# Performance work log

Hardware: AMD Instinct MI355X
Metric: run time of the kernel (lower is better)

## Reference

```python
import jax, jax.numpy as jnp
import numpy as np

EMBED = 1024
HEADS = 16
HEAD_DIM = EMBED // HEADS


def setup_inputs() -> dict:
    key = jax.random.key(0)
    kx, kq, kk, kv, ko = jax.random.split(key, 5)
    s = 1.0 / np.sqrt(EMBED)
    return {
        "x": jax.random.normal(kx, (4, 2048, EMBED), dtype=jnp.float32),
        "Wq": jax.random.uniform(kq, (EMBED, EMBED), jnp.float32, -s, s),
        "Wk": jax.random.uniform(kk, (EMBED, EMBED), jnp.float32, -s, s),
        "Wv": jax.random.uniform(kv, (EMBED, EMBED), jnp.float32, -s, s),
        "Wo": jax.random.uniform(ko, (EMBED, EMBED), jnp.float32, -s, s),
    }


def reference(x, Wq, Wk, Wv, Wo):
    B, S, E = x.shape
    # nn.Linear computes x @ W.T; weights stored as (out, in)
    q = (x @ Wq.T).reshape(B, S, HEADS, HEAD_DIM).transpose(0, 2, 1, 3)  # [B,H,S,D]
    k = (x @ Wk.T).reshape(B, S, HEADS, HEAD_DIM).transpose(0, 2, 1, 3)
    v = (x @ Wv.T).reshape(B, S, HEADS, HEAD_DIM).transpose(0, 2, 1, 3)
    scores = jnp.einsum("bhsd,bhtd->bhst", q, k) / np.sqrt(HEAD_DIM)  # [B,H,S,S]
    causal = jnp.triu(jnp.ones((S, S), dtype=bool), k=1)
    scores = jnp.where(causal[None, None], -jnp.inf, scores)
    probs = jax.nn.softmax(scores, axis=-1)  # dropout_rate=0 -> identity
    attn = jnp.einsum("bhst,bhtd->bhsd", probs, v)  # [B,H,S,D]
    attn = attn.transpose(0, 2, 1, 3).reshape(B, S, E)
    return attn @ Wo.T
```

## Files before the change

### kernel.cpp

```cpp
#include <hip/hip_runtime.h>

#define EMB 1024
#define NHEADS 16
#define HD 64
#define BATCH 4
#define SEQ 2048
#define MTOK (BATCH*SEQ)

typedef __bf16 bf16x8 __attribute__((ext_vector_type(8)));
typedef __bf16 bf16x4 __attribute__((ext_vector_type(4)));
typedef float  f32x4  __attribute__((ext_vector_type(4)));

#define MFMA16(a,b,c) __builtin_amdgcn_mfma_f32_16x16x32_bf16(a,b,c,0,0,0)

__device__ __forceinline__ void gload_lds16(const __bf16* g, __bf16* l) {
    __builtin_amdgcn_global_load_lds(
        (__attribute__((address_space(1))) void*)(g),
        (__attribute__((address_space(3))) void*)(l), 16, 0, 0);
}

__global__ void cvt_f32_bf16(const float* __restrict__ in, __bf16* __restrict__ out, int n) {
    int i = (blockIdx.x * blockDim.x + threadIdx.x) * 4;
    if (i < n) {
        float4 v = *(const float4*)(in + i);
        bf16x4 o = { (__bf16)v.x, (__bf16)v.y, (__bf16)v.z, (__bf16)v.w };
        *(bf16x4*)(out + i) = o;
    }
}

__device__ __forceinline__ void gemm_bt_body(
    const __bf16* __restrict__ A, const __bf16* __restrict__ Bw,
    int tileM, int tileN, __bf16* As, __bf16* Bs, f32x4 acc[4][4])
{
    const int tid   = threadIdx.x;
    const int w     = tid >> 6;
    const int lane  = tid & 63;
    const int mlane = lane & 15;
    const int quad  = lane >> 4;
    const int wm    = (w >> 1) * 64;
    const int wn    = (w & 1) * 64;

    const f32x4 fzero = {0.f, 0.f, 0.f, 0.f};
    #pragma unroll
    for (int mi = 0; mi < 4; ++mi)
        #pragma unroll
        for (int ni = 0; ni < 4; ++ni) acc[mi][ni] = fzero;

    for (int kt = 0; kt < EMB; kt += 32) {
        #pragma unroll
        for (int i = 0; i < 2; ++i) {
            int cbase = i * 256 + w * 64;
            int c  = cbase + lane;
            int m  = c >> 2;
            int dq = (c & 3) ^ ((m >> 1) & 3);
            gload_lds16(A  + (size_t)(tileM + m) * EMB + kt + dq * 8, As + cbase * 8);
            gload_lds16(Bw + (size_t)(tileN + m) * EMB + kt + dq * 8, Bs + cbase * 8);
        }
        asm volatile("s_waitcnt vmcnt(0)" ::: "memory");
        __syncthreads();

        bf16x8 af[4], bfr[4];
        #pragma unroll
        for (int mi = 0; mi < 4; ++mi) {
            int row = wm + mi * 16 + mlane;
            af[mi] = *(const bf16x8*)(As + row * 32 + ((quad ^ ((row >> 1) & 3)) * 8));
        }
        #pragma unroll
        for (int ni = 0; ni < 4; ++ni) {
            int row = wn + ni * 16 + mlane;
            bfr[ni] = *(const bf16x8*)(Bs + row * 32 + ((quad ^ ((row >> 1) & 3)) * 8));
        }
        #pragma unroll
        for (int mi = 0; mi < 4; ++mi)
            #pragma unroll
            for (int ni = 0; ni < 4; ++ni)
                acc[mi][ni] = MFMA16(af[mi], bfr[ni], acc[mi][ni]);
        __syncthreads();
    }
}

__global__ __launch_bounds__(256) void qkv_gemm(
    const __bf16* __restrict__ xb,
    const __bf16* __restrict__ wq, const __bf16* __restrict__ wk, const __bf16* __restrict__ wv,
    __bf16* __restrict__ Qb, __bf16* __restrict__ Kb, __bf16* __restrict__ Vb)
{
    __shared__ __bf16 As[128 * 32];
    __shared__ __bf16 Bs[128 * 32];
    const int z = blockIdx.z;
    const __bf16* W = (z == 0) ? wq : (z == 1) ? wk : wv;
    __bf16* O       = (z == 0) ? Qb : (z == 1) ? Kb : Vb;
    const float scl = (z == 0) ? 0.18033688011112042f : 1.0f;

    f32x4 acc[4][4];
    gemm_bt_body(xb, W, blockIdx.y * 128, blockIdx.x * 128, As, Bs, acc);

    const int tid = threadIdx.x, w = tid >> 6, lane = tid & 63;
    const int mlane = lane & 15, quad = lane >> 4;
    const int wm = (w >> 1) * 64, wn = (w & 1) * 64;
    #pragma unroll
    for (int mi = 0; mi < 4; ++mi) {
        #pragma unroll
        for (int ni = 0; ni < 4; ++ni) {
            int ncol = blockIdx.x * 128 + wn + ni * 16 + mlane;
            int h = ncol >> 6, d = ncol & 63;
            #pragma unroll
            for (int r = 0; r < 4; ++r) {
                int mr = blockIdx.y * 128 + wm + mi * 16 + quad * 4 + r;
                int b = mr >> 11, s = mr & 2047;
                O[(((size_t)b * NHEADS + h) * SEQ + s) * HD + d] = (__bf16)(acc[mi][ni][r] * scl);
            }
        }
    }
}

__global__ __launch_bounds__(256) void out_gemm(
    const __bf16* __restrict__ attnb, const __bf16* __restrict__ wo, float* __restrict__ out)
{
    __shared__ __bf16 As[128 * 32];
    __shared__ __bf16 Bs[128 * 32];
    f32x4 acc[4][4];
    gemm_bt_body(attnb, wo, blockIdx.y * 128, blockIdx.x * 128, As, Bs, acc);

    const int tid = threadIdx.x, w = tid >> 6, lane = tid & 63;
    const int mlane = lane & 15, quad = lane >> 4;
    const int wm = (w >> 1) * 64, wn = (w & 1) * 64;
    #pragma unroll
    for (int mi = 0; mi < 4; ++mi) {
        #pragma unroll
        for (int ni = 0; ni < 4; ++ni) {
            int ncol = blockIdx.x * 128 + wn + ni * 16 + mlane;
            #pragma unroll
            for (int r = 0; r < 4; ++r) {
                int mr = blockIdx.y * 128 + wm + mi * 16 + quad * 4 + r;
                out[(size_t)mr * EMB + ncol] = acc[mi][ni][r];
            }
        }
    }
}

__global__ __launch_bounds__(256, 2) void attn_kernel(
    const __bf16* __restrict__ Qb, const __bf16* __restrict__ Kb,
    const __bf16* __restrict__ Vb, __bf16* __restrict__ attnb)
{
    __shared__ __bf16 Ks[64 * 72];
    __shared__ __bf16 Vt[8 * 520];
    __shared__ __bf16 Ps[4 * 32 * 72];

    const int tid = threadIdx.x, w = tid >> 6, lane = tid & 63;
    const int mlane = lane & 15, quad = lane >> 4;
    const int h = blockIdx.y, b = blockIdx.z;
    const size_t headoff = ((size_t)b * NHEADS + h) * SEQ * HD;
    const __bf16* Qg = Qb + headoff;
    const __bf16* Kg = Kb + headoff;
    const __bf16* Vg = Vb + headoff;
    __bf16* Psw = Ps + w * 32 * 72;

    const int st_t = lane;
    const int st_d = w * 16;

    for (int sp = 0; sp < 2; ++sp) {
        const int strip = sp ? (15 - blockIdx.x) : blockIdx.x;
        const int qbase = strip * 128;
        const int qw    = qbase + w * 32;

        bf16x8 bq[2][2];
        #pragma unroll
        for (int nt = 0; nt < 2; ++nt)
            #pragma unroll
            for (int ks = 0; ks < 2; ++ks)
                bq[nt][ks] = *(const bf16x8*)(Qg + (size_t)(qw + nt * 16 + mlane) * HD + ks * 32 + quad * 8);

        float m_run[2] = {-3e38f, -3e38f};
        float l_run[2] = {0.f, 0.f};
        f32x4 o[2][4];
        const f32x4 fzero = {0.f, 0.f, 0.f, 0.f};
        #pragma unroll
        for (int qt = 0; qt < 2; ++qt)
            #pragma unroll
            for (int dt = 0; dt < 4; ++dt) o[qt][dt] = fzero;

        const int nch = qbase / 64 + 2;
        for (int c = 0; c < nch; ++c) {
            const int tb = c * 64;
            __syncthreads();
            {
                const __bf16* kp = Kg + (size_t)(tb + st_t) * HD + st_d;
                bf16x8 k0 = *(const bf16x8*)kp;
                bf16x8 k1 = *(const bf16x8*)(kp + 8);
                *(bf16x8*)(Ks + st_t * 72 + st_d)     = k0;
                *(bf16x8*)(Ks + st_t * 72 + st_d + 8) = k1;
                const __bf16* vp = Vg + (size_t)(tb + st_t) * HD + st_d;
                bf16x8 v0 = *(const bf16x8*)vp;
                bf16x8 v1 = *(const bf16x8*)(vp + 8);
                __bf16* vd = Vt + (st_t >> 3) * 520 + (st_t & 7);
                #pragma unroll
                for (int j = 0; j < 8; ++j) vd[(st_d + j) * 8]     = v0[j];
                #pragma unroll
                for (int j = 0; j < 8; ++j) vd[(st_d + 8 + j) * 8] = v1[j];
            }
            __syncthreads();
            if (tb > qw + 31) continue;

            f32x4 s[4][2];
            #pragma unroll
            for (int mt = 0; mt < 4; ++mt) {
                bf16x8 ak0 = *(const bf16x8*)(Ks + (mt * 16 + mlane) * 72 + quad * 8);
                bf16x8 ak1 = *(const bf16x8*)(Ks + (mt * 16 + mlane) * 72 + 32 + quad * 8);
                f32x4 z = fzero;
                s[mt][0] = MFMA16(ak1, bq[0][1], MFMA16(ak0, bq[0][0], z));
                s[mt][1] = MFMA16(ak1, bq[1][1], MFMA16(ak0, bq[1][0], z));
            }

            if (tb + 63 > qw) {
                #pragma unroll
                for (int nt = 0; nt < 2; ++nt) {
                    int qrel = qw + nt * 16 + mlane - tb - quad * 4;
                    #pragma unroll
                    for (int mt = 0; mt < 4; ++mt)
                        #pragma unroll
                        for (int r = 0; r < 4; ++r)
                            if (mt * 16 + r > qrel) s[mt][nt][r] = -3e38f;
                }
            }

            float alpha[2];
            #pragma unroll
            for (int nt = 0; nt < 2; ++nt) {
                float mx = s[0][nt][0];
                #pragma unroll
                for (int mt = 0; mt < 4; ++mt)
                    #pragma unroll
                    for (int r = 0; r < 4; ++r) mx = fmaxf(mx, s[mt][nt][r]);
                mx = fmaxf(mx, __shfl_xor(mx, 16));
                mx = fmaxf(mx, __shfl_xor(mx, 32));
                float mnew = fmaxf(m_run[nt], mx);
                alpha[nt]  = __builtin_amdgcn_exp2f(m_run[nt] - mnew);
                m_run[nt]  = mnew;

                f32x4 ps4 = fzero;
                #pragma unroll
                for (int mt = 0; mt < 4; ++mt) {
                    #pragma unroll
                    for (int r = 0; r < 4; ++r)
                        s[mt][nt][r] = __builtin_amdgcn_exp2f(s[mt][nt][r] - mnew);
                    ps4 += s[mt][nt];
                    bf16x4 pb = { (__bf16)s[mt][nt][0], (__bf16)s[mt][nt][1],
                                  (__bf16)s[mt][nt][2], (__bf16)s[mt][nt][3] };
                    *(bf16x4*)(Psw + (nt * 16 + mlane) * 72 + mt * 16 + quad * 4) = pb;
                }
                float rs = (ps4[0] + ps4[1]) + (ps4[2] + ps4[3]);
                rs += __shfl_xor(rs, 16);
                rs += __shfl_xor(rs, 32);
                l_run[nt] = l_run[nt] * alpha[nt] + rs;
            }

            #pragma unroll
            for (int qt = 0; qt < 2; ++qt)
                #pragma unroll
                for (int r = 0; r < 4; ++r) {
                    float ar = __shfl(alpha[qt], quad * 4 + r);
                    #pragma unroll
                    for (int dt = 0; dt < 4; ++dt) o[qt][dt][r] *= ar;
                }

            bf16x8 ap[2][2];
            #pragma unroll
            for (int qt = 0; qt < 2; ++qt)
                #pragma unroll
                for (int ks = 0; ks < 2; ++ks)
                    ap[qt][ks] = *(const bf16x8*)(Psw + (qt * 16 + mlane) * 72 + ks * 32 + quad * 8);
            #pragma unroll
            for (int ks = 0; ks < 2; ++ks)
                #pragma unroll
                for (int dt = 0; dt < 4; ++dt) {
                    bf16x8 bv = *(const bf16x8*)(Vt + (ks * 4 + quad) * 520 + (dt * 16 + mlane) * 8);
                    #pragma unroll
                    for (int qt = 0; qt < 2; ++qt)
                        o[qt][dt] = MFMA16(ap[qt][ks], bv, o[qt][dt]);
                }
        }

        #pragma unroll
        for (int qt = 0; qt < 2; ++qt)
            #pragma unroll
            for (int r = 0; r < 4; ++r) {
                float lr = __shfl(l_run[qt], quad * 4 + r);
                float linv = 1.0f / lr;
                int q = qw + qt * 16 + quad * 4 + r;
                size_t rowoff = ((size_t)b * SEQ + q) * EMB + h * HD;
                #pragma unroll
                for (int dt = 0; dt < 4; ++dt)
                    attnb[rowoff + dt * 16 + mlane] = (__bf16)(o[qt][dt][r] * linv);
            }
    }
}

extern "C" void kernel_launch(void* const* d_in, const int* in_sizes, int n_in,
                              void* d_out, int out_size, void* d_ws, size_t ws_size,
                              hipStream_t stream) {
    const float* x  = (const float*)d_in[0];
    const float* Wq = (const float*)d_in[1];
    const float* Wk = (const float*)d_in[2];
    const float* Wv = (const float*)d_in[3];
    const float* Wo = (const float*)d_in[4];
    float* out = (float*)d_out;

    char* ws = (char*)d_ws;
    __bf16* xb    = (__bf16*)(ws);
    __bf16* wqb   = (__bf16*)(ws + 16777216);
    __bf16* wkb   = (__bf16*)(ws + 18874368);
    __bf16* wvb   = (__bf16*)(ws + 20971520);
    __bf16* wob   = (__bf16*)(ws + 23068672);
    __bf16* qb    = (__bf16*)(ws + 25165824);
    __bf16* kb    = (__bf16*)(ws + 41943040);
    __bf16* vb    = (__bf16*)(ws + 58720256);
    __bf16* attnb = (__bf16*)(ws + 75497472);

    cvt_f32_bf16<<<8192, 256, 0, stream>>>(x,  xb,  MTOK * EMB);
    cvt_f32_bf16<<<1024, 256, 0, stream>>>(Wq, wqb, EMB * EMB);
    cvt_f32_bf16<<<1024, 256, 0, stream>>>(Wk, wkb, EMB * EMB);
    cvt_f32_bf16<<<1024, 256, 0, stream>>>(Wv, wvb, EMB * EMB);
    cvt_f32_bf16<<<1024, 256, 0, stream>>>(Wo, wob, EMB * EMB);

    qkv_gemm<<<dim3(EMB / 128, MTOK / 128, 3), 256, 0, stream>>>(xb, wqb, wkb, wvb, qb, kb, vb);

    attn_kernel<<<dim3(8, NHEADS, BATCH), 256, 0, stream>>>(qb, kb, vb, attnb);

    out_gemm<<<dim3(EMB / 128, MTOK / 128, 1), 256, 0, stream>>>(attnb, wob, out);
}
```

Baseline: 282.4 us.

## Double-buffer K via async LDS loads, shrink attention query tiles, fuse conversions

The attention kernel now loads the next K chunk straight into a second XOR-swizzled LDS buffer with global_load_lds and prefetches V into registers. This overlaps global loads with the current chunk's compute. Each wave now handles 16 query rows instead of 32, the grid doubles to 16 strip pairs, and launch bounds allow 4 blocks per CU, all aimed at finer causal balance and higher occupancy. Causal work skipping is now finer-grained, skipping whole 16-key MFMA tiles, and the five fp32-to-bf16 conversion launches are merged into one. The cost is less K/V reuse per loaded chunk, more blocks, and many grid slots in the merged conversion that do nothing.

```diff
diff --git a/kernel.cpp b/kernel.cpp
--- a/kernel.cpp
+++ b/kernel.cpp
@@ -19,12 +19,19 @@
         (__attribute__((address_space(3))) void*)(l), 16, 0, 0);
 }
 
-__global__ void cvt_f32_bf16(const float* __restrict__ in, __bf16* __restrict__ out, int n) {
+__global__ void cvt_all(const float* __restrict__ x,  const float* __restrict__ wq,
+                        const float* __restrict__ wk, const float* __restrict__ wv,
+                        const float* __restrict__ wo,
+                        __bf16* xb, __bf16* wqb, __bf16* wkb, __bf16* wvb, __bf16* wob) {
+    int z = blockIdx.y;
+    const float* src = (z == 0) ? x : (z == 1) ? wq : (z == 2) ? wk : (z == 3) ? wv : wo;
+    __bf16*      dst = (z == 0) ? xb : (z == 1) ? wqb : (z == 2) ? wkb : (z == 3) ? wvb : wob;
+    int n = (z == 0) ? MTOK * EMB : EMB * EMB;
     int i = (blockIdx.x * blockDim.x + threadIdx.x) * 4;
     if (i < n) {
-        float4 v = *(const float4*)(in + i);
+        float4 v = *(const float4*)(src + i);
         bf16x4 o = { (__bf16)v.x, (__bf16)v.y, (__bf16)v.z, (__bf16)v.w };
-        *(bf16x4*)(out + i) = o;
+        *(bf16x4*)(dst + i) = o;
     }
 }
 
@@ -138,13 +145,13 @@
     }
 }
 
-__global__ __launch_bounds__(256, 2) void attn_kernel(
+__global__ __launch_bounds__(256, 4) void attn_kernel(
     const __bf16* __restrict__ Qb, const __bf16* __restrict__ Kb,
     const __bf16* __restrict__ Vb, __bf16* __restrict__ attnb)
 {
-    __shared__ __bf16 Ks[64 * 72];
+    __shared__ __bf16 Ks[2 * 64 * 64];
     __shared__ __bf16 Vt[8 * 520];
-    __shared__ __bf16 Ps[4 * 32 * 72];
+    __shared__ __bf16 Ps[4 * 16 * 72];
 
     const int tid = threadIdx.x, w = tid >> 6, lane = tid & 63;
     const int mlane = lane & 15, quad = lane >> 4;
@@ -153,145 +160,163 @@
     const __bf16* Qg = Qb + headoff;
     const __bf16* Kg = Kb + headoff;
     const __bf16* Vg = Vb + headoff;
-    __bf16* Psw = Ps + w * 32 * 72;
-
-    const int st_t = lane;
-    const int st_d = w * 16;
+    __bf16* Psw = Ps + w * 16 * 72;
+    const int g0 = quad ^ (mlane & 7);
+    const f32x4 fzero = {0.f, 0.f, 0.f, 0.f};
 
     for (int sp = 0; sp < 2; ++sp) {
-        const int strip = sp ? (15 - blockIdx.x) : blockIdx.x;
-        const int qbase = strip * 128;
-        const int qw    = qbase + w * 32;
-
-        bf16x8 bq[2][2];
-        #pragma unroll
-        for (int nt = 0; nt < 2; ++nt)
-            #pragma unroll
-            for (int ks = 0; ks < 2; ++ks)
-                bq[nt][ks] = *(const bf16x8*)(Qg + (size_t)(qw + nt * 16 + mlane) * HD + ks * 32 + quad * 8);
-
-        float m_run[2] = {-3e38f, -3e38f};
-        float l_run[2] = {0.f, 0.f};
-        f32x4 o[2][4];
-        const f32x4 fzero = {0.f, 0.f, 0.f, 0.f};
-        #pragma unroll
-        for (int qt = 0; qt < 2; ++qt)
-            #pragma unroll
-            for (int dt = 0; dt < 4; ++dt) o[qt][dt] = fzero;
-
-        const int nch = qbase / 64 + 2;
+        const int strip = sp ? (31 - (int)blockIdx.x) : (int)blockIdx.x;
+        const int qw  = strip * 64 + w * 16;
+        const int nch = strip + 1;
+
+        __syncthreads();
+
+        #pragma unroll
+        for (int i = 0; i < 2; ++i) {
+            int cb = w * 64 + i * 256;
+            int c_ = cb + lane;
+            int row = c_ >> 3;
+            int scol = (c_ & 7) ^ (row & 7);
+            gload_lds16(Kg + (size_t)row * HD + scol * 8, Ks + cb * 8);
+        }
+        bf16x8 vr0, vr1, vr0n, vr1n;
+        {
+            const __bf16* vp = Vg + (size_t)lane * HD + w * 16;
+            vr0 = *(const bf16x8*)vp;
+            vr1 = *(const bf16x8*)(vp + 8);
+        }
+        bf16x8 bq0 = *(const bf16x8*)(Qg + (size_t)(qw + mlane) * HD + quad * 8);
+        bf16x8 bq1 = *(const bf16x8*)(Qg + (size_t)(qw + mlane) * HD + 32 + quad * 8);
+
+        float m_run = -3e38f, l_run = 0.f;
+        f32x4 o[4];
+        #pragma unroll
+        for (int dt = 0; dt < 4; ++dt) o[dt] = fzero;
+
         for (int c = 0; c < nch; ++c) {
             const int tb = c * 64;
+            const __bf16* Kp = Ks + (c & 1) * 4096;
+            __bf16*       Kn = Ks + ((c & 1) ^ 1) * 4096;
+
             __syncthreads();
             {
-                const __bf16* kp = Kg + (size_t)(tb + st_t) * HD + st_d;
-                bf16x8 k0 = *(const bf16x8*)kp;
-                bf16x8 k1 = *(const bf16x8*)(kp + 8);
-                *(bf16x8*)(Ks + st_t * 72 + st_d)     = k0;
-                *(bf16x8*)(Ks + st_t * 72 + st_d + 8) = k1;
-                const __bf16* vp = Vg + (size_t)(tb + st_t) * HD + st_d;
-                bf16x8 v0 = *(const bf16x8*)vp;
-                bf16x8 v1 = *(const bf16x8*)(vp + 8);
-                __bf16* vd = Vt + (st_t >> 3) * 520 + (st_t & 7);
-                #pragma unroll
-                for (int j = 0; j < 8; ++j) vd[(st_d + j) * 8]     = v0[j];
-                #pragma unroll
-                for (int j = 0; j < 8; ++j) vd[(st_d + 8 + j) * 8] = v1[j];
-            }
+                __bf16* vd = Vt + (lane >> 3) * 520 + (lane & 7);
+                int rot = lane & 7;
+                #pragma unroll
+                for (int j = 0; j < 8; ++j) { int jj = (j + rot) & 7; vd[(w * 16 + jj) * 8] = vr0[jj]; }
+                #pragma unroll
+                for (int j = 0; j < 8; ++j) { int jj = (j + rot) & 7; vd[(w * 16 + 8 + jj) * 8] = vr1[jj]; }
+            }
+            asm volatile("s_waitcnt vmcnt(0)" ::: "memory");
             __syncthreads();
-            if (tb > qw + 31) continue;
-
-            f32x4 s[4][2];
-            #pragma unroll
-            for (int mt = 0; mt < 4; ++mt) {
-                bf16x8 ak0 = *(const bf16x8*)(Ks + (mt * 16 + mlane) * 72 + quad * 8);
-                bf16x8 ak1 = *(const bf16x8*)(Ks + (mt * 16 + mlane) * 72 + 32 + quad * 8);
-                f32x4 z = fzero;
-                s[mt][0] = MFMA16(ak1, bq[0][1], MFMA16(ak0, bq[0][0], z));
-                s[mt][1] = MFMA16(ak1, bq[1][1], MFMA16(ak0, bq[1][0], z));
-            }
-
-            if (tb + 63 > qw) {
-                #pragma unroll
-                for (int nt = 0; nt < 2; ++nt) {
-                    int qrel = qw + nt * 16 + mlane - tb - quad * 4;
+
+            if (c + 1 < nch) {
+                const int tbn = tb + 64;
+                #pragma unroll
+                for (int i = 0; i < 2; ++i) {
+                    int cb = w * 64 + i * 256;
+                    int c_ = cb + lane;
+                    int row = c_ >> 3;
+                    int scol = (c_ & 7) ^ (row & 7);
+                    gload_lds16(Kg + (size_t)(tbn + row) * HD + scol * 8, Kn + cb * 8);
+                }
+                const __bf16* vp = Vg + (size_t)(tbn + lane) * HD + w * 16;
+                vr0n = *(const bf16x8*)vp;
+                vr1n = *(const bf16x8*)(vp + 8);
+            }
+
+            const int rel = qw + 15 - tb;
+            {
+                const int kv  = rel < 63 ? rel : 63;
+                const int nmt = (kv >> 4) + 1;
+                const int nks = (kv >> 5) + 1;
+
+                f32x4 s[4];
+                #pragma unroll
+                for (int mt = 0; mt < 4; ++mt) {
+                    if (mt < nmt) {
+                        const __bf16* ka = Kp + (mt * 16 + mlane) * 64;
+                        bf16x8 ak0 = *(const bf16x8*)(ka + g0 * 8);
+                        bf16x8 ak1 = *(const bf16x8*)(ka + (g0 ^ 4) * 8);
+                        s[mt] = MFMA16(ak1, bq1, MFMA16(ak0, bq0, fzero));
+                    }
+                }
+                if (rel < 78) {
+                    const int qrel = qw + mlane - tb - quad * 4;
                     #pragma unroll
-                    for (int mt = 0; mt < 4; ++mt)
+                    for (int mt = 0; mt < 4; ++mt) if (mt < nmt)
                         #pragma unroll
                         for (int r = 0; r < 4; ++r)
-                            if (mt * 16 + r > qrel) s[mt][nt][r] = -3e38f;
-                }
-            }
-
-            float alpha[2];
-            #pragma unroll
-            for (int nt = 0; nt < 2; ++nt) {
-                float mx = s[0][nt][0];
-                #pragma unroll
-                for (int mt = 0; mt < 4; ++mt)
+                            if (mt * 16 + r > qrel) s[mt][r] = -3e38f;
+                }
+
+                f32x4 vmax = s[0];
+                #pragma unroll
+                for (int mt = 1; mt < 4; ++mt) if (mt < nmt) {
                     #pragma unroll
-                    for (int r = 0; r < 4; ++r) mx = fmaxf(mx, s[mt][nt][r]);
+                    for (int r = 0; r < 4; ++r) vmax[r] = fmaxf(vmax[r], s[mt][r]);
+                }
+                float mx = fmaxf(fmaxf(vmax[0], vmax[1]), fmaxf(vmax[2], vmax[3]));
                 mx = fmaxf(mx, __shfl_xor(mx, 16));
                 mx = fmaxf(mx, __shfl_xor(mx, 32));
-                float mnew = fmaxf(m_run[nt], mx);
-                alpha[nt]  = __builtin_amdgcn_exp2f(m_run[nt] - mnew);
-                m_run[nt]  = mnew;
-
-                f32x4 ps4 = fzero;
+                float mnew  = fmaxf(m_run, mx);
+                float alpha = __builtin_amdgcn_exp2f(m_run - mnew);
+                m_run = mnew;
+
+                f32x4 vsum = fzero;
                 #pragma unroll
                 for (int mt = 0; mt < 4; ++mt) {
-                    #pragma unroll
-                    for (int r = 0; r < 4; ++r)
-                        s[mt][nt][r] = __builtin_amdgcn_exp2f(s[mt][nt][r] - mnew);
-                    ps4 += s[mt][nt];
-                    bf16x4 pb = { (__bf16)s[mt][nt][0], (__bf16)s[mt][nt][1],
-                                  (__bf16)s[mt][nt][2], (__bf16)s[mt][nt][3] };
-                    *(bf16x4*)(Psw + (nt * 16 + mlane) * 72 + mt * 16 + quad * 4) = pb;
-                }
-                float rs = (ps4[0] + ps4[1]) + (ps4[2] + ps4[3]);
+                    if (mt < nmt) {
+                        #pragma unroll
+                        for (int r = 0; r < 4; ++r)
+                            s[mt][r] = __builtin_amdgcn_exp2f(s[mt][r] - mnew);
+                        vsum += s[mt];
+                        bf16x4 pb = { (__bf16)s[mt][0], (__bf16)s[mt][1],
+                                      (__bf16)s[mt][2], (__bf16)s[mt][3] };
+                        *(bf16x4*)(Psw + mlane * 72 + mt * 16 + quad * 4) = pb;
+                    } else if (mt < 2 * nks) {
+                        bf16x4 zb = { (__bf16)0.f, (__bf16)0.f, (__bf16)0.f, (__bf16)0.f };
+                        *(bf16x4*)(Psw + mlane * 72 + mt * 16 + quad * 4) = zb;
+                    }
+                }
+                float rs = (vsum[0] + vsum[1]) + (vsum[2] + vsum[3]);
                 rs += __shfl_xor(rs, 16);
                 rs += __shfl_xor(rs, 32);
-                l_run[nt] = l_run[nt] * alpha[nt] + rs;
-            }
-
+                l_run = l_run * alpha + rs;
+
+                float ar[4];
+                #pragma unroll
+                for (int r = 0; r < 4; ++r) ar[r] = __shfl(alpha, quad * 4 + r);
+                #pragma unroll
+                for (int dt = 0; dt < 4; ++dt)
+                    #pragma unroll
+                    for (int r = 0; r < 4; ++r) o[dt][r] *= ar[r];
+
+                #pragma unroll
+                for (int ks = 0; ks < 2; ++ks) {
+                    if (ks < nks) {
+                        bf16x8 ap = *(const bf16x8*)(Psw + mlane * 72 + ks * 32 + quad * 8);
+                        #pragma unroll
+                        for (int dt = 0; dt < 4; ++dt) {
+                            bf16x8 bv = *(const bf16x8*)(Vt + (ks * 4 + quad) * 520 + (dt * 16 + mlane) * 8);
+                            o[dt] = MFMA16(ap, bv, o[dt]);
+                        }
+                    }
+                }
+            }
+            vr0 = vr0n; vr1 = vr1n;
+        }
+
+        #pragma unroll
+        for (int r = 0; r < 4; ++r) {
+            float lr = __shfl(l_run, quad * 4 + r);
+            float linv = 1.0f / lr;
+            int q = qw + quad * 4 + r;
+            size_t rowoff = ((size_t)b * SEQ + q) * EMB + h * HD;
             #pragma unroll
-            for (int qt = 0; qt < 2; ++qt)
-                #pragma unroll
-                for (int r = 0; r < 4; ++r) {
-                    float ar = __shfl(alpha[qt], quad * 4 + r);
-                    #pragma unroll
-                    for (int dt = 0; dt < 4; ++dt) o[qt][dt][r] *= ar;
-                }
-
-            bf16x8 ap[2][2];
-            #pragma unroll
-            for (int qt = 0; qt < 2; ++qt)
-                #pragma unroll
-                for (int ks = 0; ks < 2; ++ks)
-                    ap[qt][ks] = *(const bf16x8*)(Psw + (qt * 16 + mlane) * 72 + ks * 32 + quad * 8);
-            #pragma unroll
-            for (int ks = 0; ks < 2; ++ks)
-                #pragma unroll
-                for (int dt = 0; dt < 4; ++dt) {
-                    bf16x8 bv = *(const bf16x8*)(Vt + (ks * 4 + quad) * 520 + (dt * 16 + mlane) * 8);
-                    #pragma unroll
-                    for (int qt = 0; qt < 2; ++qt)
-                        o[qt][dt] = MFMA16(ap[qt][ks], bv, o[qt][dt]);
-                }
-        }
-
-        #pragma unroll
-        for (int qt = 0; qt < 2; ++qt)
-            #pragma unroll
-            for (int r = 0; r < 4; ++r) {
-                float lr = __shfl(l_run[qt], quad * 4 + r);
-                float linv = 1.0f / lr;
-                int q = qw + qt * 16 + quad * 4 + r;
-                size_t rowoff = ((size_t)b * SEQ + q) * EMB + h * HD;
-                #pragma unroll
-                for (int dt = 0; dt < 4; ++dt)
-                    attnb[rowoff + dt * 16 + mlane] = (__bf16)(o[qt][dt][r] * linv);
-            }
+            for (int dt = 0; dt < 4; ++dt)
+                attnb[rowoff + dt * 16 + mlane] = (__bf16)(o[dt][r] * linv);
+        }
     }
 }
 
@@ -316,15 +341,11 @@
     __bf16* vb    = (__bf16*)(ws + 58720256);
     __bf16* attnb = (__bf16*)(ws + 75497472);
 
-    cvt_f32_bf16<<<8192, 256, 0, stream>>>(x,  xb,  MTOK * EMB);
-    cvt_f32_bf16<<<1024, 256, 0, stream>>>(Wq, wqb, EMB * EMB);
-    cvt_f32_bf16<<<1024, 256, 0, stream>>>(Wk, wkb, EMB * EMB);
-    cvt_f32_bf16<<<1024, 256, 0, stream>>>(Wv, wvb, EMB * EMB);
-    cvt_f32_bf16<<<1024, 256, 0, stream>>>(Wo, wob, EMB * EMB);
+    cvt_all<<<dim3(8192, 5), 256, 0, stream>>>(x, Wq, Wk, Wv, Wo, xb, wqb, wkb, wvb, wob);
 
     qkv_gemm<<<dim3(EMB / 128, MTOK / 128, 3), 256, 0, stream>>>(xb, wqb, wkb, wvb, qb, kb, vb);
 
-    attn_kernel<<<dim3(8, NHEADS, BATCH), 256, 0, stream>>>(qb, kb, vb, attnb);
+    attn_kernel<<<dim3(16, NHEADS, BATCH), 256, 0, stream>>>(qb, kb, vb, attnb);
 
     out_gemm<<<dim3(EMB / 128, MTOK / 128, 1), 256, 0, stream>>>(attnb, wob, out);
 }
```

Measured after the change: 328.4 us. +16.3%, slower.
